# Kernel tuning notes

Hardware: AMD Instinct MI355X
Metric: run time of the kernel (lower is better)

The kernel has to match this reference:

```python
import jax, jax.numpy as jnp
import numpy as np

E = 1024   # embed_size
H = 16     # num_heads
D = E // H # head_dim
B, S = 4, 2048

def setup_inputs() -> dict:
    key = jax.random.key(0)
    ks = jax.random.split(key, 11)
    scale = 1.0 / np.sqrt(E)
    inp = {
        "Q": jax.random.normal(ks[0], (B, S, E), jnp.float32),
        "K": jax.random.normal(ks[1], (B, S, E), jnp.float32),
        "V": jax.random.normal(ks[2], (B, S, E), jnp.float32),
        "Wq": jax.random.uniform(ks[3], (E, E), jnp.float32, -scale, scale),
        "bq": jax.random.uniform(ks[4], (E,), jnp.float32, -scale, scale),
        "Wk": jax.random.uniform(ks[5], (E, E), jnp.float32, -scale, scale),
        "bk": jax.random.uniform(ks[6], (E,), jnp.float32, -scale, scale),
        "Wv": jax.random.uniform(ks[7], (E, E), jnp.float32, -scale, scale),
        "bv": jax.random.uniform(ks[8], (E,), jnp.float32, -scale, scale),
        "Wo": jax.random.uniform(ks[9], (E, E), jnp.float32, -scale, scale),
        "bo": jax.random.uniform(ks[10], (E,), jnp.float32, -scale, scale),
    }
    return inp

def reference(Q, K, V, Wq, bq, Wk, bk, Wv, bv, Wo, bo):
    b, sq, _ = Q.shape
    sk = K.shape[1]
    # Linear projections (torch Linear: x @ W.T + b), split into heads -> (b, H, s, D)
    q = (Q @ Wq.T + bq).reshape(b, sq, H, D).transpose(0, 2, 1, 3)
    k = (K @ Wk.T + bk).reshape(b, sk, H, D).transpose(0, 2, 1, 3)
    v = (V @ Wv.T + bv).reshape(b, sk, H, D).transpose(0, 2, 1, 3)
    scores = jnp.einsum('bhqd,bhkd->bhqk', q, k) / jnp.sqrt(jnp.float32(D))
    attn = jax.nn.softmax(scores, axis=-1)
    out = jnp.einsum('bhqk,bhkd->bhqd', attn, v)  # (b, H, sq, D)
    concat = out.transpose(0, 2, 1, 3).reshape(b, sq, E)
    return concat @ Wo.T + bo
```

## Files before the change

kernel.cpp:

```cpp
#include <hip/hip_runtime.h>
#include <hip/hip_bf16.h>

typedef unsigned short u16;
typedef unsigned int u32;
typedef __bf16 bf16x8 __attribute__((ext_vector_type(8)));
typedef float f32x4 __attribute__((ext_vector_type(4)));
typedef float f32x16 __attribute__((ext_vector_type(16)));
typedef unsigned int u32x2 __attribute__((ext_vector_type(2)));

constexpr int E_ = 1024, H_ = 16, D_ = 64, B_ = 4, S_ = 2048;
constexpr int GM = B_ * S_;
constexpr int GN = E_;
constexpr int GK = E_;

__device__ __forceinline__ u16 f2bf(float f) {
  union { float f; u32 u; } v; v.f = f;
  u32 r = v.u + 0x7fffu + ((v.u >> 16) & 1u);
  return (u16)(r >> 16);
}

__device__ __forceinline__ bf16x8 ld_bf16x8(const u16* p) {
  return *reinterpret_cast<const bf16x8*>(p);
}

__device__ __forceinline__ f32x4 mfma16(bf16x8 a, bf16x8 b, f32x4 c) {
  return __builtin_amdgcn_mfma_f32_16x16x32_bf16(a, b, c, 0, 0, 0);
}
__device__ __forceinline__ f32x16 mfma32(bf16x8 a, bf16x8 b, f32x16 c) {
  return __builtin_amdgcn_mfma_f32_32x32x16_bf16(a, b, c, 0, 0, 0);
}

__device__ __forceinline__ u32 cvtpk(float lo, float hi) {
  u32 r;
  asm("v_cvt_pk_bf16_f32 %0, %1, %2" : "=v"(r) : "v"(lo), "v"(hi));
  return r;
}

__device__ __forceinline__ void pl32swap(u32& a, u32& b) {
#if __has_builtin(__builtin_amdgcn_permlane32_swap)
  u32x2 r = __builtin_amdgcn_permlane32_swap(a, b, false, false);
  a = r.x; b = r.y;
#else
  asm volatile("v_permlane32_swap_b32 %0, %1" : "+v"(a), "+v"(b));
#endif
}

__device__ __forceinline__ float fexp2(float x) {
#if __has_builtin(__builtin_amdgcn_exp2f)
  return __builtin_amdgcn_exp2f(x);
#else
  return exp2f(x);
#endif
}

#define GLOAD_LDS16(gp, lp)                                                       \
  __builtin_amdgcn_global_load_lds(                                               \
      (const __attribute__((address_space(1))) u32*)(const void*)(gp),            \
      (__attribute__((address_space(3))) u32*)(void*)(lp), 16, 0, 0)

__global__ __launch_bounds__(256) void cvt7(
    const float4* __restrict__ s0, const float4* __restrict__ s1,
    const float4* __restrict__ s2, const float4* __restrict__ s3,
    const float4* __restrict__ s4, const float4* __restrict__ s5,
    const float4* __restrict__ s6,
    ushort4* __restrict__ d0, ushort4* __restrict__ d1,
    ushort4* __restrict__ d2, ushort4* __restrict__ d3,
    ushort4* __restrict__ d4, ushort4* __restrict__ d5,
    ushort4* __restrict__ d6) {
  long i = (long)blockIdx.x * 256 + threadIdx.x;
  const float4* s; ushort4* d; long j;
  if (i < 2097152L)      { s = s0; d = d0; j = i; }
  else if (i < 4194304L) { s = s1; d = d1; j = i - 2097152L; }
  else if (i < 6291456L) { s = s2; d = d2; j = i - 4194304L; }
  else if (i < 6553600L) { s = s3; d = d3; j = i - 6291456L; }
  else if (i < 6815744L) { s = s4; d = d4; j = i - 6553600L; }
  else if (i < 7077888L) { s = s5; d = d5; j = i - 6815744L; }
  else                   { s = s6; d = d6; j = i - 7077888L; }
  float4 v = s[j];
  ushort4 o;
  o.x = f2bf(v.x); o.y = f2bf(v.y); o.z = f2bf(v.z); o.w = f2bf(v.w);
  d[j] = o;
}

template <int MODE>
__global__ __launch_bounds__(256, 2) void gemm_bt(
    const u16* __restrict__ A, const u16* __restrict__ Bw,
    const float* __restrict__ bias, void* __restrict__ Cout, float scale) {
  __shared__ u16 As[128 * 32];
  __shared__ u16 Bs[128 * 32];
  const int tid = threadIdx.x;
  const int lane = tid & 63, w = tid >> 6;
  const int lr = lane & 15, lg = lane >> 4;
  const int bn = blockIdx.x, bm = blockIdx.y;
  const int wm = (w >> 1) * 64, wn = (w & 1) * 64;

  f32x4 acc[4][4] = {};

  const int byte0 = (w * 2 + 0) * 1024 + lane * 16;
  const int byte1 = (w * 2 + 1) * 1024 + lane * 16;
  const int r0 = byte0 >> 6, c0 = (byte0 & 63) >> 1;
  const int r1 = byte1 >> 6, c1 = (byte1 & 63) >> 1;
  const u16* Arow0 = A + (size_t)(bm * 128 + r0) * GK + c0;
  const u16* Arow1 = A + (size_t)(bm * 128 + r1) * GK + c1;
  const u16* Brow0 = Bw + (size_t)(bn * 128 + r0) * GK + c0;
  const u16* Brow1 = Bw + (size_t)(bn * 128 + r1) * GK + c1;
  u16* As0 = &As[(w * 2 + 0) * 512];
  u16* As1 = &As[(w * 2 + 1) * 512];
  u16* Bs0 = &Bs[(w * 2 + 0) * 512];
  u16* Bs1 = &Bs[(w * 2 + 1) * 512];

  for (int kt = 0; kt < GK / 32; ++kt) {
    const int ko = kt * 32;
    GLOAD_LDS16(Arow0 + ko, As0);
    GLOAD_LDS16(Arow1 + ko, As1);
    GLOAD_LDS16(Brow0 + ko, Bs0);
    GLOAD_LDS16(Brow1 + ko, Bs1);
    __syncthreads();
    bf16x8 af[4], bf_[4];
#pragma unroll
    for (int mi = 0; mi < 4; ++mi)
      af[mi] = ld_bf16x8(&As[(wm + mi * 16 + lr) * 32 + lg * 8]);
#pragma unroll
    for (int ni = 0; ni < 4; ++ni)
      bf_[ni] = ld_bf16x8(&Bs[(wn + ni * 16 + lr) * 32 + lg * 8]);
#pragma unroll
    for (int mi = 0; mi < 4; ++mi)
#pragma unroll
      for (int ni = 0; ni < 4; ++ni)
        acc[mi][ni] = mfma16(af[mi], bf_[ni], acc[mi][ni]);
    __syncthreads();
  }

#pragma unroll
  for (int mi = 0; mi < 4; ++mi)
#pragma unroll
    for (int ni = 0; ni < 4; ++ni) {
      const int n = bn * 128 + wn + ni * 16 + lr;
      const float bv = bias[n];
#pragma unroll
      for (int r = 0; r < 4; ++r) {
        const int m = bm * 128 + wm + mi * 16 + lg * 4 + r;
        const float vv = (acc[mi][ni][r] + bv) * scale;
        if (MODE == 0) {
          const int b = m >> 11, s = m & 2047, h = n >> 6, d = n & 63;
          ((u16*)Cout)[(((size_t)(b * 16 + h) * 2048 + s) * 64) + d] = f2bf(vv);
        } else if (MODE == 1) {
          const int b = m >> 11, s = m & 2047, h = n >> 6, d = n & 63;
          ((u16*)Cout)[((size_t)(b * 16 + h) * 64 + d) * 2048 + s] = f2bf(vv);
        } else {
          ((float*)Cout)[(size_t)m * 1024 + n] = vv;
        }
      }
    }
}

__global__ __launch_bounds__(256, 2) void attn2(
    const u16* __restrict__ q, const u16* __restrict__ k,
    const u16* __restrict__ vT, u16* __restrict__ concat) {
  __shared__ u16 KT[2][64 * 64];
  __shared__ u16 VTl[2][64 * 64];
  const int tid = threadIdx.x, lane = tid & 63, w = tid >> 6;
  const int l31 = lane & 31, hi = lane >> 5;
  const int qt = blockIdx.x, bh = blockIdx.y;
  const u16* qbp = q + (size_t)bh * S_ * D_;
  const char* kbase = (const char*)(k + (size_t)bh * S_ * D_);
  const char* vbase = (const char*)(vT + (size_t)bh * D_ * S_);
  const int q0 = qt * 256 + w * 64;

  bf16x8 qf[2][4];
#pragma unroll
  for (int qs = 0; qs < 2; ++qs)
#pragma unroll
    for (int kc = 0; kc < 4; ++kc)
      qf[qs][kc] =
          ld_bf16x8(&qbp[(size_t)(q0 + qs * 32 + l31) * 64 + kc * 16 + hi * 8]);

  f32x16 acc[2][2] = {};
  float m_[2] = {-1e30f, -1e30f}, l_[2] = {0.f, 0.f};

  const int srow = w * 8 + (lane >> 3);
  const int cswz = (((lane & 7) ^ (lane >> 3)) << 4);
  const char* gk0 = kbase + (size_t)srow * 128 + cswz;
  const char* gk1 = kbase + (size_t)(32 + srow) * 128 + cswz;
  const char* gv0 = vbase + (size_t)srow * (S_ * 2) + cswz;
  const char* gv1 = vbase + (size_t)(32 + srow) * (S_ * 2) + cswz;

  int col4[4];
#pragma unroll
  for (int c = 0; c < 4; ++c)
    col4[c] = (((c * 32 + hi * 16) ^ ((lane & 7) << 4)) >> 1);
  const int rrow = l31 * 64;

#define STAGE(t, buf)                                                     \
  do {                                                                    \
    GLOAD_LDS16(gk0 + (size_t)(t) * 8192, &KT[buf][(0 * 4 + w) * 512]);   \
    GLOAD_LDS16(gk1 + (size_t)(t) * 8192, &KT[buf][(1 * 4 + w) * 512]);   \
    GLOAD_LDS16(gv0 + (size_t)(t) * 128, &VTl[buf][(0 * 4 + w) * 512]);   \
    GLOAD_LDS16(gv1 + (size_t)(t) * 128, &VTl[buf][(1 * 4 + w) * 512]);   \
  } while (0)

  STAGE(0, 0);
  asm volatile("s_waitcnt vmcnt(0)" ::: "memory");
  __syncthreads();

  for (int t = 0; t < S_ / 64; ++t) {
    const int cur = t & 1, nxt = cur ^ 1;
    if (t < S_ / 64 - 1) STAGE(t + 1, nxt);

    f32x16 sF[2][2] = {};
#pragma unroll
    for (int st = 0; st < 2; ++st)
#pragma unroll
      for (int kc = 0; kc < 4; ++kc) {
        bf16x8 kf = ld_bf16x8(&KT[cur][st * 2048 + rrow + col4[kc]]);
        sF[0][st] = mfma32(kf, qf[0][kc], sF[0][st]);
        sF[1][st] = mfma32(kf, qf[1][kc], sF[1][st]);
      }

#pragma unroll
    for (int qs = 0; qs < 2; ++qs) {
      float tm = sF[qs][0][0];
#pragma unroll
      for (int e = 1; e < 16; ++e) tm = fmaxf(tm, sF[qs][0][e]);
#pragma unroll
      for (int e = 0; e < 16; ++e) tm = fmaxf(tm, sF[qs][1][e]);
      u32 ta = __builtin_bit_cast(u32, tm), tb = ta;
      pl32swap(ta, tb);
      tm = fmaxf(__builtin_bit_cast(float, ta), __builtin_bit_cast(float, tb));
      if (!__all(tm <= m_[qs] + 8.0f)) {
        const float mn = fmaxf(m_[qs], tm);
        const float csc = fexp2(m_[qs] - mn);
        m_[qs] = mn;
        l_[qs] *= csc;
#pragma unroll
        for (int dt = 0; dt < 2; ++dt)
#pragma unroll
          for (int e = 0; e < 16; ++e) acc[qs][dt][e] *= csc;
      }
      float ps = 0.f;
#pragma unroll
      for (int st = 0; st < 2; ++st)
#pragma unroll
        for (int e = 0; e < 16; ++e) {
          const float p = fexp2(sF[qs][st][e] - m_[qs]);
          sF[qs][st][e] = p;
          ps += p;
        }
      u32 sa = __builtin_bit_cast(u32, ps), sb = sa;
      pl32swap(sa, sb);
      l_[qs] += __builtin_bit_cast(float, sa) + __builtin_bit_cast(float, sb);
    }

#pragma unroll
    for (int ks = 0; ks < 4; ++ks) {
      bf16x8 vt0 = ld_bf16x8(&VTl[cur][rrow + col4[ks]]);
      bf16x8 vt1 = ld_bf16x8(&VTl[cur][2048 + rrow + col4[ks]]);
#pragma unroll
      for (int qs = 0; qs < 2; ++qs) {
        const int st = ks >> 1, b = (ks & 1) * 8;
        u32 w0 = cvtpk(sF[qs][st][b + 0], sF[qs][st][b + 1]);
        u32 w1 = cvtpk(sF[qs][st][b + 2], sF[qs][st][b + 3]);
        u32 w2 = cvtpk(sF[qs][st][b + 4], sF[qs][st][b + 5]);
        u32 w3 = cvtpk(sF[qs][st][b + 6], sF[qs][st][b + 7]);
        pl32swap(w0, w2);
        pl32swap(w1, w3);
        union { u32 u[4]; bf16x8 v; } pa;
        pa.u[0] = w0; pa.u[1] = w1; pa.u[2] = w2; pa.u[3] = w3;
        acc[qs][0] = mfma32(vt0, pa.v, acc[qs][0]);
        acc[qs][1] = mfma32(vt1, pa.v, acc[qs][1]);
      }
    }

    asm volatile("s_waitcnt vmcnt(0)" ::: "memory");
    __syncthreads();
  }
#undef STAGE

  const int b = bh >> 4, h = bh & 15;
#pragma unroll
  for (int qs = 0; qs < 2; ++qs) {
    const float inv = 1.f / l_[qs];
    const int s = q0 + qs * 32 + l31;
    u16* crow = concat + ((size_t)(b * 2048 + s)) * 1024 + h * 64;
#pragma unroll
    for (int dt = 0; dt < 2; ++dt)
#pragma unroll
      for (int g = 0; g < 4; ++g) {
        ushort4 o;
        o.x = f2bf(acc[qs][dt][g * 4 + 0] * inv);
        o.y = f2bf(acc[qs][dt][g * 4 + 1] * inv);
        o.z = f2bf(acc[qs][dt][g * 4 + 2] * inv);
        o.w = f2bf(acc[qs][dt][g * 4 + 3] * inv);
        *(ushort4*)&crow[dt * 32 + g * 8 + hi * 4] = o;
      }
  }
}

extern "C" void kernel_launch(void* const* d_in, const int* in_sizes, int n_in,
                              void* d_out, int out_size, void* d_ws,
                              size_t ws_size, hipStream_t stream) {
  const float* Qf = (const float*)d_in[0];
  const float* Kf = (const float*)d_in[1];
  const float* Vf = (const float*)d_in[2];
  const float* Wq = (const float*)d_in[3];
  const float* bq = (const float*)d_in[4];
  const float* Wk = (const float*)d_in[5];
  const float* bk = (const float*)d_in[6];
  const float* Wv = (const float*)d_in[7];
  const float* bv = (const float*)d_in[8];
  const float* Wo = (const float*)d_in[9];
  const float* bo = (const float*)d_in[10];

  char* ws = (char*)d_ws;
  u16* Xq = (u16*)(ws);
  u16* Xk = (u16*)(ws + (size_t)16777216);
  u16* Xv = (u16*)(ws + (size_t)2 * 16777216);
  u16* Wqb = (u16*)(ws + (size_t)3 * 16777216);
  u16* Wkb = Wqb + 1048576;
  u16* Wvb = Wkb + 1048576;
  u16* Wob = Wvb + 1048576;
  u16* qb = (u16*)(ws + (size_t)3 * 16777216 + 8388608);
  u16* kb = qb + (size_t)GM * GN;
  u16* vTb = kb + (size_t)GM * GN;
  u16* concat = Xq;

  cvt7<<<28672, 256, 0, stream>>>(
      (const float4*)Qf, (const float4*)Kf, (const float4*)Vf,
      (const float4*)Wq, (const float4*)Wk, (const float4*)Wv,
      (const float4*)Wo, (ushort4*)Xq, (ushort4*)Xk, (ushort4*)Xv,
      (ushort4*)Wqb, (ushort4*)Wkb, (ushort4*)Wvb, (ushort4*)Wob);

  dim3 gg(GN / 128, GM / 128);
  gemm_bt<0><<<gg, 256, 0, stream>>>(Xq, Wqb, bq, qb, 0.18033688011112042f);
  gemm_bt<0><<<gg, 256, 0, stream>>>(Xk, Wkb, bk, kb, 1.0f);
  gemm_bt<1><<<gg, 256, 0, stream>>>(Xv, Wvb, bv, vTb, 1.0f);

  attn2<<<dim3(S_ / 256, B_ * H_), 256, 0, stream>>>(qb, kb, vTb, concat);

  gemm_bt<2><<<gg, 256, 0, stream>>>(concat, Wob, bo, d_out, 1.0f);
}
```

Before: 232.5 us.

## Fuse QKV projections into one launch and halve attention rows per wave

Merges the three Q/K/V projection GEMMs into a single grid of 192x8 blocks that picks its input, weight, bias and output layout from the block row. The attention kernel now gives each wave 32 query rows instead of 64, which doubles the grid and cuts register use so four blocks can fit per CU. The row-sum cross-lane reduction moves out of the loop to the epilogue, and the max and sum reductions use several independent accumulators. The aim is to reduce launch overhead and tail effects and to raise occupancy for better latency hiding, at the cost of re-reading K/V tiles twice as often.

```diff
diff --git a/kernel.cpp b/kernel.cpp
--- a/kernel.cpp
+++ b/kernel.cpp
@@ -82,10 +82,86 @@
   d[j] = o;
 }
 
-template <int MODE>
-__global__ __launch_bounds__(256, 2) void gemm_bt(
+__global__ __launch_bounds__(256, 3) void gemm_qkv(
+    const u16* __restrict__ Xbase, const u16* __restrict__ Wbase,
+    const float* __restrict__ bq, const float* __restrict__ bk,
+    const float* __restrict__ bv, u16* __restrict__ Obase, float qscale) {
+  __shared__ u16 As[128 * 32];
+  __shared__ u16 Bs[128 * 32];
+  const int tid = threadIdx.x;
+  const int lane = tid & 63, w = tid >> 6;
+  const int lr = lane & 15, lg = lane >> 4;
+  const int bn = blockIdx.x, bm = blockIdx.y;
+  const int sel = bm >> 6, bml = bm & 63;
+  const int wm = (w >> 1) * 64, wn = (w & 1) * 64;
+
+  const u16* A = Xbase + (size_t)sel * 8388608;
+  const u16* Bw = Wbase + (size_t)sel * 1048576;
+  const float* bias = sel == 0 ? bq : (sel == 1 ? bk : bv);
+  const float scale = sel == 0 ? qscale : 1.0f;
+
+  f32x4 acc[4][4] = {};
+
+  const int byte0 = (w * 2 + 0) * 1024 + lane * 16;
+  const int byte1 = (w * 2 + 1) * 1024 + lane * 16;
+  const int r0 = byte0 >> 6, c0 = (byte0 & 63) >> 1;
+  const int r1 = byte1 >> 6, c1 = (byte1 & 63) >> 1;
+  const u16* Arow0 = A + (size_t)(bml * 128 + r0) * GK + c0;
+  const u16* Arow1 = A + (size_t)(bml * 128 + r1) * GK + c1;
+  const u16* Brow0 = Bw + (size_t)(bn * 128 + r0) * GK + c0;
+  const u16* Brow1 = Bw + (size_t)(bn * 128 + r1) * GK + c1;
+  u16* As0 = &As[(w * 2 + 0) * 512];
+  u16* As1 = &As[(w * 2 + 1) * 512];
+  u16* Bs0 = &Bs[(w * 2 + 0) * 512];
+  u16* Bs1 = &Bs[(w * 2 + 1) * 512];
+
+  for (int kt = 0; kt < GK / 32; ++kt) {
+    const int ko = kt * 32;
+    GLOAD_LDS16(Arow0 + ko, As0);
+    GLOAD_LDS16(Arow1 + ko, As1);
+    GLOAD_LDS16(Brow0 + ko, Bs0);
+    GLOAD_LDS16(Brow1 + ko, Bs1);
+    __syncthreads();
+    bf16x8 af[4], bf_[4];
+#pragma unroll
+    for (int mi = 0; mi < 4; ++mi)
+      af[mi] = ld_bf16x8(&As[(wm + mi * 16 + lr) * 32 + lg * 8]);
+#pragma unroll
+    for (int ni = 0; ni < 4; ++ni)
+      bf_[ni] = ld_bf16x8(&Bs[(wn + ni * 16 + lr) * 32 + lg * 8]);
+#pragma unroll
+    for (int mi = 0; mi < 4; ++mi)
+#pragma unroll
+      for (int ni = 0; ni < 4; ++ni)
+        acc[mi][ni] = mfma16(af[mi], bf_[ni], acc[mi][ni]);
+    __syncthreads();
+  }
+
+#pragma unroll
+  for (int mi = 0; mi < 4; ++mi)
+#pragma unroll
+    for (int ni = 0; ni < 4; ++ni) {
+      const int n = bn * 128 + wn + ni * 16 + lr;
+      const float bv_ = bias[n];
+#pragma unroll
+      for (int r = 0; r < 4; ++r) {
+        const int m = bml * 128 + wm + mi * 16 + lg * 4 + r;
+        const float vv = (acc[mi][ni][r] + bv_) * scale;
+        const int b = m >> 11, s = m & 2047, h = n >> 6, d = n & 63;
+        if (sel < 2) {
+          u16* O = Obase + (size_t)sel * 8388608;
+          O[(((size_t)(b * 16 + h) * 2048 + s) * 64) + d] = f2bf(vv);
+        } else {
+          u16* O = Obase + (size_t)2 * 8388608;
+          O[((size_t)(b * 16 + h) * 64 + d) * 2048 + s] = f2bf(vv);
+        }
+      }
+    }
+}
+
+__global__ __launch_bounds__(256, 2) void gemm_wo(
     const u16* __restrict__ A, const u16* __restrict__ Bw,
-    const float* __restrict__ bias, void* __restrict__ Cout, float scale) {
+    const float* __restrict__ bias, float* __restrict__ Cout) {
   __shared__ u16 As[128 * 32];
   __shared__ u16 Bs[128 * 32];
   const int tid = threadIdx.x;
@@ -140,21 +216,12 @@
 #pragma unroll
       for (int r = 0; r < 4; ++r) {
         const int m = bm * 128 + wm + mi * 16 + lg * 4 + r;
-        const float vv = (acc[mi][ni][r] + bv) * scale;
-        if (MODE == 0) {
-          const int b = m >> 11, s = m & 2047, h = n >> 6, d = n & 63;
-          ((u16*)Cout)[(((size_t)(b * 16 + h) * 2048 + s) * 64) + d] = f2bf(vv);
-        } else if (MODE == 1) {
-          const int b = m >> 11, s = m & 2047, h = n >> 6, d = n & 63;
-          ((u16*)Cout)[((size_t)(b * 16 + h) * 64 + d) * 2048 + s] = f2bf(vv);
-        } else {
-          ((float*)Cout)[(size_t)m * 1024 + n] = vv;
-        }
+        Cout[(size_t)m * 1024 + n] = acc[mi][ni][r] + bv;
       }
     }
 }
 
-__global__ __launch_bounds__(256, 2) void attn2(
+__global__ __launch_bounds__(256, 4) void attn3(
     const u16* __restrict__ q, const u16* __restrict__ k,
     const u16* __restrict__ vT, u16* __restrict__ concat) {
   __shared__ u16 KT[2][64 * 64];
@@ -165,18 +232,15 @@
   const u16* qbp = q + (size_t)bh * S_ * D_;
   const char* kbase = (const char*)(k + (size_t)bh * S_ * D_);
   const char* vbase = (const char*)(vT + (size_t)bh * D_ * S_);
-  const int q0 = qt * 256 + w * 64;
-
-  bf16x8 qf[2][4];
-#pragma unroll
-  for (int qs = 0; qs < 2; ++qs)
-#pragma unroll
-    for (int kc = 0; kc < 4; ++kc)
-      qf[qs][kc] =
-          ld_bf16x8(&qbp[(size_t)(q0 + qs * 32 + l31) * 64 + kc * 16 + hi * 8]);
-
-  f32x16 acc[2][2] = {};
-  float m_[2] = {-1e30f, -1e30f}, l_[2] = {0.f, 0.f};
+  const int q0 = qt * 128 + w * 32;
+
+  bf16x8 qf[4];
+#pragma unroll
+  for (int kc = 0; kc < 4; ++kc)
+    qf[kc] = ld_bf16x8(&qbp[(size_t)(q0 + l31) * 64 + kc * 16 + hi * 8]);
+
+  f32x16 acc[2] = {};
+  float m_ = -1e30f, l_ = 0.f;
 
   const int srow = w * 8 + (lane >> 3);
   const int cswz = (((lane & 7) ^ (lane >> 3)) << 4);
@@ -207,68 +271,70 @@
     const int cur = t & 1, nxt = cur ^ 1;
     if (t < S_ / 64 - 1) STAGE(t + 1, nxt);
 
-    f32x16 sF[2][2] = {};
+    f32x16 sF[2] = {};
 #pragma unroll
     for (int st = 0; st < 2; ++st)
 #pragma unroll
       for (int kc = 0; kc < 4; ++kc) {
         bf16x8 kf = ld_bf16x8(&KT[cur][st * 2048 + rrow + col4[kc]]);
-        sF[0][st] = mfma32(kf, qf[0][kc], sF[0][st]);
-        sF[1][st] = mfma32(kf, qf[1][kc], sF[1][st]);
+        sF[st] = mfma32(kf, qf[kc], sF[st]);
       }
 
-#pragma unroll
-    for (int qs = 0; qs < 2; ++qs) {
-      float tm = sF[qs][0][0];
-#pragma unroll
-      for (int e = 1; e < 16; ++e) tm = fmaxf(tm, sF[qs][0][e]);
-#pragma unroll
-      for (int e = 0; e < 16; ++e) tm = fmaxf(tm, sF[qs][1][e]);
-      u32 ta = __builtin_bit_cast(u32, tm), tb = ta;
-      pl32swap(ta, tb);
-      tm = fmaxf(__builtin_bit_cast(float, ta), __builtin_bit_cast(float, tb));
-      if (!__all(tm <= m_[qs] + 8.0f)) {
-        const float mn = fmaxf(m_[qs], tm);
-        const float csc = fexp2(m_[qs] - mn);
-        m_[qs] = mn;
-        l_[qs] *= csc;
-#pragma unroll
-        for (int dt = 0; dt < 2; ++dt)
-#pragma unroll
-          for (int e = 0; e < 16; ++e) acc[qs][dt][e] *= csc;
+    float a0 = fmaxf(sF[0][0], sF[1][0]);
+    float a1 = fmaxf(sF[0][1], sF[1][1]);
+    float a2 = fmaxf(sF[0][2], sF[1][2]);
+    float a3 = fmaxf(sF[0][3], sF[1][3]);
+#pragma unroll
+    for (int e = 4; e < 16; e += 4) {
+      a0 = fmaxf(a0, fmaxf(sF[0][e + 0], sF[1][e + 0]));
+      a1 = fmaxf(a1, fmaxf(sF[0][e + 1], sF[1][e + 1]));
+      a2 = fmaxf(a2, fmaxf(sF[0][e + 2], sF[1][e + 2]));
+      a3 = fmaxf(a3, fmaxf(sF[0][e + 3], sF[1][e + 3]));
+    }
+    float tm = fmaxf(fmaxf(a0, a1), fmaxf(a2, a3));
+    u32 ta = __builtin_bit_cast(u32, tm), tb = ta;
+    pl32swap(ta, tb);
+    tm = fmaxf(__builtin_bit_cast(float, ta), __builtin_bit_cast(float, tb));
+    if (!__all(tm <= m_ + 8.0f)) {
+      const float mn = fmaxf(m_, tm);
+      const float csc = fexp2(m_ - mn);
+      m_ = mn;
+      l_ *= csc;
+#pragma unroll
+      for (int dt = 0; dt < 2; ++dt)
+#pragma unroll
+        for (int e = 0; e < 16; ++e) acc[dt][e] *= csc;
+    }
+    float s0 = 0.f, s1 = 0.f, s2 = 0.f, s3 = 0.f;
+#pragma unroll
+    for (int st = 0; st < 2; ++st)
+#pragma unroll
+      for (int e = 0; e < 16; e += 4) {
+        const float p0 = fexp2(sF[st][e + 0] - m_);
+        const float p1 = fexp2(sF[st][e + 1] - m_);
+        const float p2 = fexp2(sF[st][e + 2] - m_);
+        const float p3 = fexp2(sF[st][e + 3] - m_);
+        sF[st][e + 0] = p0; sF[st][e + 1] = p1;
+        sF[st][e + 2] = p2; sF[st][e + 3] = p3;
+        s0 += p0; s1 += p1; s2 += p2; s3 += p3;
       }
-      float ps = 0.f;
-#pragma unroll
-      for (int st = 0; st < 2; ++st)
-#pragma unroll
-        for (int e = 0; e < 16; ++e) {
-          const float p = fexp2(sF[qs][st][e] - m_[qs]);
-          sF[qs][st][e] = p;
-          ps += p;
-        }
-      u32 sa = __builtin_bit_cast(u32, ps), sb = sa;
-      pl32swap(sa, sb);
-      l_[qs] += __builtin_bit_cast(float, sa) + __builtin_bit_cast(float, sb);
-    }
+    l_ += (s0 + s1) + (s2 + s3);
 
 #pragma unroll
     for (int ks = 0; ks < 4; ++ks) {
       bf16x8 vt0 = ld_bf16x8(&VTl[cur][rrow + col4[ks]]);
       bf16x8 vt1 = ld_bf16x8(&VTl[cur][2048 + rrow + col4[ks]]);
-#pragma unroll
-      for (int qs = 0; qs < 2; ++qs) {
-        const int st = ks >> 1, b = (ks & 1) * 8;
-        u32 w0 = cvtpk(sF[qs][st][b + 0], sF[qs][st][b + 1]);
-        u32 w1 = cvtpk(sF[qs][st][b + 2], sF[qs][st][b + 3]);
-        u32 w2 = cvtpk(sF[qs][st][b + 4], sF[qs][st][b + 5]);
-        u32 w3 = cvtpk(sF[qs][st][b + 6], sF[qs][st][b + 7]);
-        pl32swap(w0, w2);
-        pl32swap(w1, w3);
-        union { u32 u[4]; bf16x8 v; } pa;
-        pa.u[0] = w0; pa.u[1] = w1; pa.u[2] = w2; pa.u[3] = w3;
-        acc[qs][0] = mfma32(vt0, pa.v, acc[qs][0]);
-        acc[qs][1] = mfma32(vt1, pa.v, acc[qs][1]);
-      }
+      const int st = ks >> 1, b = (ks & 1) * 8;
+      u32 w0 = cvtpk(sF[st][b + 0], sF[st][b + 1]);
+      u32 w1 = cvtpk(sF[st][b + 2], sF[st][b + 3]);
+      u32 w2 = cvtpk(sF[st][b + 4], sF[st][b + 5]);
+      u32 w3 = cvtpk(sF[st][b + 6], sF[st][b + 7]);
+      pl32swap(w0, w2);
+      pl32swap(w1, w3);
+      union { u32 u[4]; bf16x8 v; } pa;
+      pa.u[0] = w0; pa.u[1] = w1; pa.u[2] = w2; pa.u[3] = w3;
+      acc[0] = mfma32(vt0, pa.v, acc[0]);
+      acc[1] = mfma32(vt1, pa.v, acc[1]);
     }
 
     asm volatile("s_waitcnt vmcnt(0)" ::: "memory");
@@ -276,24 +342,25 @@
   }
 #undef STAGE
 
+  u32 la = __builtin_bit_cast(u32, l_), lb = la;
+  pl32swap(la, lb);
+  const float lt =
+      __builtin_bit_cast(float, la) + __builtin_bit_cast(float, lb);
+  const float inv = 1.f / lt;
   const int b = bh >> 4, h = bh & 15;
-#pragma unroll
-  for (int qs = 0; qs < 2; ++qs) {
-    const float inv = 1.f / l_[qs];
-    const int s = q0 + qs * 32 + l31;
-    u16* crow = concat + ((size_t)(b * 2048 + s)) * 1024 + h * 64;
-#pragma unroll
-    for (int dt = 0; dt < 2; ++dt)
-#pragma unroll
-      for (int g = 0; g < 4; ++g) {
-        ushort4 o;
-        o.x = f2bf(acc[qs][dt][g * 4 + 0] * inv);
-        o.y = f2bf(acc[qs][dt][g * 4 + 1] * inv);
-        o.z = f2bf(acc[qs][dt][g * 4 + 2] * inv);
-        o.w = f2bf(acc[qs][dt][g * 4 + 3] * inv);
-        *(ushort4*)&crow[dt * 32 + g * 8 + hi * 4] = o;
-      }
-  }
+  const int s = q0 + l31;
+  u16* crow = concat + ((size_t)(b * 2048 + s)) * 1024 + h * 64;
+#pragma unroll
+  for (int dt = 0; dt < 2; ++dt)
+#pragma unroll
+    for (int g = 0; g < 4; ++g) {
+      ushort4 o;
+      o.x = f2bf(acc[dt][g * 4 + 0] * inv);
+      o.y = f2bf(acc[dt][g * 4 + 1] * inv);
+      o.z = f2bf(acc[dt][g * 4 + 2] * inv);
+      o.w = f2bf(acc[dt][g * 4 + 3] * inv);
+      *(ushort4*)&crow[dt * 32 + g * 8 + hi * 4] = o;
+    }
 }
 
 extern "C" void kernel_launch(void* const* d_in, const int* in_sizes, int n_in,
@@ -313,12 +380,8 @@
 
   char* ws = (char*)d_ws;
   u16* Xq = (u16*)(ws);
-  u16* Xk = (u16*)(ws + (size_t)16777216);
-  u16* Xv = (u16*)(ws + (size_t)2 * 16777216);
   u16* Wqb = (u16*)(ws + (size_t)3 * 16777216);
-  u16* Wkb = Wqb + 1048576;
-  u16* Wvb = Wkb + 1048576;
-  u16* Wob = Wvb + 1048576;
+  u16* Wob = Wqb + 3 * 1048576;
   u16* qb = (u16*)(ws + (size_t)3 * 16777216 + 8388608);
   u16* kb = qb + (size_t)GM * GN;
   u16* vTb = kb + (size_t)GM * GN;
@@ -327,15 +390,15 @@
   cvt7<<<28672, 256, 0, stream>>>(
       (const float4*)Qf, (const float4*)Kf, (const float4*)Vf,
       (const float4*)Wq, (const float4*)Wk, (const float4*)Wv,
-      (const float4*)Wo, (ushort4*)Xq, (ushort4*)Xk, (ushort4*)Xv,
-      (ushort4*)Wqb, (ushort4*)Wkb, (ushort4*)Wvb, (ushort4*)Wob);
-
-  dim3 gg(GN / 128, GM / 128);
-  gemm_bt<0><<<gg, 256, 0, stream>>>(Xq, Wqb, bq, qb, 0.18033688011112042f);
-  gemm_bt<0><<<gg, 256, 0, stream>>>(Xk, Wkb, bk, kb, 1.0f);
-  gemm_bt<1><<<gg, 256, 0, stream>>>(Xv, Wvb, bv, vTb, 1.0f);
-
-  attn2<<<dim3(S_ / 256, B_ * H_), 256, 0, stream>>>(qb, kb, vTb, concat);
-
-  gemm_bt<2><<<gg, 256, 0, stream>>>(concat, Wob, bo, d_out, 1.0f);
-}
+      (const float4*)Wo, (ushort4*)Xq, (ushort4*)(Xq + 8388608),
+      (ushort4*)(Xq + 2 * 8388608), (ushort4*)Wqb, (ushort4*)(Wqb + 1048576),
+      (ushort4*)(Wqb + 2 * 1048576), (ushort4*)Wob);
+
+  gemm_qkv<<<dim3(8, 192), 256, 0, stream>>>(Xq, Wqb, bq, bk, bv, qb,
+                                             0.18033688011112042f);
+
+  attn3<<<dim3(S_ / 128, B_ * H_), 256, 0, stream>>>(qb, kb, vTb, concat);
+
+  gemm_wo<<<dim3(GN / 128, GM / 128), 256, 0, stream>>>(concat, Wob, bo,
+                                                        (float*)d_out);
+}
```

After: 245.5 us. 5.6% more time.
